# Optimization experiments

Measured on AMD Instinct MI355X. Metric: run time of the kernel, lower is better.

## Reference

```python
import jax, jax.numpy as jnp
import numpy as np


def setup_inputs() -> dict:
    key = jax.random.key(0)
    k1, k2 = jax.random.split(key)
    in_features, out_features, tokens = 4096, 4096, 8192
    x = jax.random.normal(k1, (tokens, in_features), dtype=jnp.float32)
    bound = 1.0 / np.sqrt(in_features)  # nn.Linear default init -> |W| <= 1
    W = jax.random.uniform(k2, (out_features, in_features), dtype=jnp.float32,
                           minval=-bound, maxval=bound)
    return {"x": x, "W": W}


def reference(x, W):
    # Forward of BinarizedLinear: y = x @ sign(W)^T (bias-free linear with
    # sign-binarized weights; the clamp_(-1,1) after sign() is a no-op).
    Wb = jnp.sign(W)  # [out, in], values in {-1, 0, +1}
    return jnp.einsum('ti,oi->to', x, Wb)  # [tokens, out]
```

## Files before the change

kernel.cpp:

```cpp
#include <hip/hip_runtime.h>
#include <hip/hip_bf16.h>
#include <stdint.h>

#define M_TOK 8192
#define N_OUT 4096
#define K_IN  4096

#define BM 256
#define BN 256
#define BKB 128
#define NT (K_IN / BKB)

typedef __attribute__((ext_vector_type(4))) int   i32x4;
typedef __attribute__((ext_vector_type(4))) float f32x4;

#define AS1 __attribute__((address_space(1)))
#define AS3 __attribute__((address_space(3)))
#define GLOAD_LDS16(g, l) \
  __builtin_amdgcn_global_load_lds((AS1 void*)(g), (AS3 void*)(l), 16, 0, 0)

#define BAR()     __builtin_amdgcn_s_barrier()
#define WAITALL() asm volatile("s_waitcnt vmcnt(0) lgkmcnt(0)" ::: "memory")
#define VMCNT8()  asm volatile("s_waitcnt vmcnt(8)" ::: "memory")
#define PRIO(p)   __builtin_amdgcn_s_setprio(p)
#define MFMAI8(a, b, c) __builtin_amdgcn_mfma_i32_16x16x64_i8((a), (b), (c), 0, 0, 0)

__global__ __launch_bounds__(256) void quant_x_i8(const float4* __restrict__ x,
                                                  int4* __restrict__ o,
                                                  float* __restrict__ scales) {
  const int row = blockIdx.x;
  const int t   = threadIdx.x;
  const float4* xr = x + (size_t)row * (K_IN / 4);
  float4 v[4];
  #pragma unroll
  for (int i = 0; i < 4; ++i) v[i] = xr[t * 4 + i];
  float m = 0.f;
  #pragma unroll
  for (int i = 0; i < 4; ++i)
    m = fmaxf(m, fmaxf(fmaxf(fabsf(v[i].x), fabsf(v[i].y)),
                       fmaxf(fabsf(v[i].z), fabsf(v[i].w))));
  #pragma unroll
  for (int off = 32; off; off >>= 1) m = fmaxf(m, __shfl_down(m, off));
  __shared__ float sm[4];
  if ((t & 63) == 0) sm[t >> 6] = m;
  __syncthreads();
  m = fmaxf(fmaxf(sm[0], sm[1]), fmaxf(sm[2], sm[3]));
  const float inv = m > 0.f ? 127.f / m : 0.f;
  if (t == 0) scales[row] = m > 0.f ? m / 127.f : 1.f;
  int q[4];
  #pragma unroll
  for (int i = 0; i < 4; ++i) {
    const int a0 = (int)rintf(v[i].x * inv);
    const int a1 = (int)rintf(v[i].y * inv);
    const int a2 = (int)rintf(v[i].z * inv);
    const int a3 = (int)rintf(v[i].w * inv);
    q[i] = (a0 & 255) | ((a1 & 255) << 8) | ((a2 & 255) << 16) | (a3 << 24);
  }
  o[(size_t)row * (K_IN / 16) + t] = make_int4(q[0], q[1], q[2], q[3]);
}

__global__ __launch_bounds__(256) void sgn_w_i8(const float4* __restrict__ w,
                                                int4* __restrict__ o, int n16) {
  int i = blockIdx.x * blockDim.x + threadIdx.x;
  int stride = gridDim.x * blockDim.x;
  for (; i < n16; i += stride) {
    int q[4];
    #pragma unroll
    for (int j = 0; j < 4; ++j) {
      float4 v = w[i * 4 + j];
      const int a0 = v.x > 0.f ? 1 : (v.x < 0.f ? -1 : 0);
      const int a1 = v.y > 0.f ? 1 : (v.y < 0.f ? -1 : 0);
      const int a2 = v.z > 0.f ? 1 : (v.z < 0.f ? -1 : 0);
      const int a3 = v.w > 0.f ? 1 : (v.w < 0.f ? -1 : 0);
      q[j] = (a0 & 255) | ((a1 & 255) << 8) | ((a2 & 255) << 16) | (a3 << 24);
    }
    o[i] = make_int4(q[0], q[1], q[2], q[3]);
  }
}

__global__ __launch_bounds__(512, 2) void bin_gemm_i8(const char* __restrict__ A,
                                                      const char* __restrict__ B,
                                                      const float* __restrict__ scales,
                                                      float* __restrict__ C) {
  __shared__ char lds[131072];

  const int tid  = threadIdx.x;
  const int w    = tid >> 6;
  const int lane = tid & 63;
  const int lr   = lane & 15;
  const int lk   = lane >> 4;
  const int wr   = w >> 2;
  const int wc   = w & 3;

  const int bm = blockIdx.x >> 4;
  const int bn = blockIdx.x & 15;

  const char* Ag = A + (size_t)bm * BM * K_IN;
  const char* Bg = B + (size_t)bn * BN * K_IN;

  const int c0 = w * 128 + lane;
  const int c1 = c0 + 64;
  const int r0 = c0 >> 3, r1 = c1 >> 3;
  const size_t g0 = (size_t)r0 * K_IN + (size_t)(((c0 ^ r0) & 7) << 4);
  const size_t g1 = (size_t)r1 * K_IN + (size_t)(((c1 ^ r1) & 7) << 4);
  const int ldsw = w * 128 * 16;

  auto stage = [&](int mat, int half, int tt) {
    const char* g = (mat ? Bg : Ag) + (size_t)half * (128 * K_IN)
                                    + (size_t)tt * BKB;
    char* l = &lds[((tt & 1) << 16) + (mat << 15) + (half << 14) + ldsw];
    GLOAD_LDS16(g + g0, l);
    GLOAD_LDS16(g + g1, l + 1024);
  };

  const int swz   = (lr & 7) << 4;
  const int a_row = (wr * 128 + lr) * 128;
  const int b_row = 32768 + (wc * 64 + lr) * 128;
  const int k0 = (lk * 16) ^ swz;
  const int k1 = (64 + lk * 16) ^ swz;

  i32x4 acc[8][4];
  #pragma unroll
  for (int m = 0; m < 8; ++m)
    #pragma unroll
    for (int n = 0; n < 4; ++n) { i32x4 z = {0, 0, 0, 0}; acc[m][n] = z; }

  stage(0, 0, 0); stage(0, 1, 0); stage(1, 0, 0); stage(1, 1, 0);
  stage(0, 0, 1); stage(0, 1, 1); stage(1, 0, 1); stage(1, 1, 1);
  VMCNT8();
  BAR();

  for (int t = 0; t < NT; ++t) {
    const char* L = &lds[(size_t)(t & 1) << 16];
    i32x4 aF[4][2], aS[4][2], bF[4][2];

    #pragma unroll
    for (int m = 0; m < 4; ++m) {
      aF[m][0] = *(const i32x4*)(L + a_row + m * 2048 + k0);
      aF[m][1] = *(const i32x4*)(L + a_row + m * 2048 + k1);
    }
    #pragma unroll
    for (int n = 0; n < 4; ++n) {
      bF[n][0] = *(const i32x4*)(L + b_row + n * 2048 + k0);
      bF[n][1] = *(const i32x4*)(L + b_row + n * 2048 + k1);
    }
    #pragma unroll
    for (int m = 0; m < 4; ++m) {
      aS[m][0] = *(const i32x4*)(L + a_row + 8192 + m * 2048 + k0);
      aS[m][1] = *(const i32x4*)(L + a_row + 8192 + m * 2048 + k1);
    }
    #pragma unroll
    for (int m = 0; m < 4; ++m)
      #pragma unroll
      for (int n = 0; n < 4; ++n) {
        acc[m][n] = MFMAI8(aF[m][0], bF[n][0], acc[m][n]);
        acc[m][n] = MFMAI8(aF[m][1], bF[n][1], acc[m][n]);
      }

    WAITALL();
    BAR();

    if (t + 2 < NT) {
      stage(1, 0, t + 2); stage(1, 1, t + 2);
      stage(0, 0, t + 2); stage(0, 1, t + 2);
    }
    PRIO(1);
    #pragma unroll
    for (int m = 0; m < 4; ++m)
      #pragma unroll
      for (int n = 0; n < 4; ++n) {
        acc[4 + m][n] = MFMAI8(aS[m][0], bF[n][0], acc[4 + m][n]);
        acc[4 + m][n] = MFMAI8(aS[m][1], bF[n][1], acc[4 + m][n]);
      }
    PRIO(0);
  }

  const int grow0 = bm * BM + wr * 128;
  float scl[8][4];
  #pragma unroll
  for (int m = 0; m < 8; ++m)
    #pragma unroll
    for (int j = 0; j < 4; ++j)
      scl[m][j] = scales[grow0 + m * 16 + lk * 4 + j];

  float* Cp = C + (size_t)grow0 * N_OUT + bn * BN + wc * 64;
  #pragma unroll
  for (int m = 0; m < 8; ++m)
    #pragma unroll
    for (int n = 0; n < 4; ++n)
      #pragma unroll
      for (int j = 0; j < 4; ++j)
        Cp[(size_t)(m * 16 + lk * 4 + j) * N_OUT + n * 16 + lr] =
            (float)acc[m][n][j] * scl[m][j];
}

__global__ __launch_bounds__(256) void fb_gemm(const float* __restrict__ x,
                                               const float* __restrict__ W,
                                               float* __restrict__ y) {
  __shared__ float xs[32][33];
  __shared__ float ws[32][33];
  const int bx = blockIdx.x;
  const int by = blockIdx.y;
  const int tx = threadIdx.x & 31;
  const int ty = threadIdx.x >> 5;
  float acc[4] = {0.f, 0.f, 0.f, 0.f};
  for (int k0 = 0; k0 < K_IN; k0 += 32) {
    #pragma unroll
    for (int i = 0; i < 4; ++i) {
      int r = ty + i * 8;
      xs[r][tx] = x[(size_t)(by * 32 + r) * K_IN + k0 + tx];
      float wv = W[(size_t)(bx * 32 + r) * K_IN + k0 + tx];
      ws[r][tx] = wv > 0.f ? 1.f : (wv < 0.f ? -1.f : 0.f);
    }
    __syncthreads();
    #pragma unroll
    for (int i = 0; i < 4; ++i) {
      int r = ty + i * 8;
      float s = acc[i];
      #pragma unroll
      for (int k = 0; k < 32; ++k) s += xs[r][k] * ws[tx][k];
      acc[i] = s;
    }
    __syncthreads();
  }
  #pragma unroll
  for (int i = 0; i < 4; ++i)
    y[(size_t)(by * 32 + ty + i * 8) * N_OUT + bx * 32 + tx] = acc[i];
}

extern "C" void kernel_launch(void* const* d_in, const int* in_sizes, int n_in,
                              void* d_out, int out_size, void* d_ws, size_t ws_size,
                              hipStream_t stream) {
  const float* x = (const float*)d_in[0];
  const float* W = (const float*)d_in[1];
  float* y = (float*)d_out;

  const size_t need = (size_t)M_TOK * K_IN + (size_t)N_OUT * K_IN
                    + (size_t)M_TOK * sizeof(float);
  if (ws_size >= need) {
    char*  xq = (char*)d_ws;
    char*  wq = xq + (size_t)M_TOK * K_IN;
    float* sc = (float*)(wq + (size_t)N_OUT * K_IN);
    quant_x_i8<<<M_TOK, 256, 0, stream>>>((const float4*)x, (int4*)xq, sc);
    sgn_w_i8<<<2048, 256, 0, stream>>>((const float4*)W, (int4*)wq,
                                       N_OUT * K_IN / 16);
    bin_gemm_i8<<<(M_TOK / BM) * (N_OUT / BN), 512, 0, stream>>>(xq, wq, sc, y);
  } else {
    dim3 g(N_OUT / 32, M_TOK / 32);
    fb_gemm<<<g, 256, 0, stream>>>(x, W, y);
  }
}
```

Before: 177.8 us.

## Software-pipeline LDS fragment loads across K halves and tiles in int8 GEMM

```diff
diff --git a/kernel.cpp b/kernel.cpp
--- a/kernel.cpp
+++ b/kernel.cpp
@@ -22,6 +22,8 @@
 #define BAR()     __builtin_amdgcn_s_barrier()
 #define WAITALL() asm volatile("s_waitcnt vmcnt(0) lgkmcnt(0)" ::: "memory")
 #define VMCNT8()  asm volatile("s_waitcnt vmcnt(8)" ::: "memory")
+#define LGKM12()  asm volatile("s_waitcnt lgkmcnt(12)" ::: "memory")
+#define SCHEDB()  __builtin_amdgcn_sched_barrier(0)
 #define PRIO(p)   __builtin_amdgcn_s_setprio(p)
 #define MFMAI8(a, b, c) __builtin_amdgcn_mfma_i32_16x16x64_i8((a), (b), (c), 0, 0, 0)
 
@@ -125,37 +127,37 @@
     #pragma unroll
     for (int n = 0; n < 4; ++n) { i32x4 z = {0, 0, 0, 0}; acc[m][n] = z; }
 
+  i32x4 aA[8], bA[4], aB[8], bB[4];
+
   stage(0, 0, 0); stage(0, 1, 0); stage(1, 0, 0); stage(1, 1, 0);
   stage(0, 0, 1); stage(0, 1, 1); stage(1, 0, 1); stage(1, 1, 1);
   VMCNT8();
   BAR();
+  {
+    const char* L0 = &lds[0];
+    #pragma unroll
+    for (int m = 0; m < 8; ++m) aA[m] = *(const i32x4*)(L0 + a_row + m * 2048 + k0);
+    #pragma unroll
+    for (int n = 0; n < 4; ++n) bA[n] = *(const i32x4*)(L0 + b_row + n * 2048 + k0);
+  }
 
   for (int t = 0; t < NT; ++t) {
-    const char* L = &lds[(size_t)(t & 1) << 16];
-    i32x4 aF[4][2], aS[4][2], bF[4][2];
-
-    #pragma unroll
-    for (int m = 0; m < 4; ++m) {
-      aF[m][0] = *(const i32x4*)(L + a_row + m * 2048 + k0);
-      aF[m][1] = *(const i32x4*)(L + a_row + m * 2048 + k1);
-    }
-    #pragma unroll
-    for (int n = 0; n < 4; ++n) {
-      bF[n][0] = *(const i32x4*)(L + b_row + n * 2048 + k0);
-      bF[n][1] = *(const i32x4*)(L + b_row + n * 2048 + k1);
-    }
-    #pragma unroll
-    for (int m = 0; m < 4; ++m) {
-      aS[m][0] = *(const i32x4*)(L + a_row + 8192 + m * 2048 + k0);
-      aS[m][1] = *(const i32x4*)(L + a_row + 8192 + m * 2048 + k1);
-    }
-    #pragma unroll
-    for (int m = 0; m < 4; ++m)
-      #pragma unroll
-      for (int n = 0; n < 4; ++n) {
-        acc[m][n] = MFMAI8(aF[m][0], bF[n][0], acc[m][n]);
-        acc[m][n] = MFMAI8(aF[m][1], bF[n][1], acc[m][n]);
-      }
+    const char* Lc = &lds[(size_t)(t & 1) << 16];
+    const char* Ln = &lds[(size_t)(~t & 1) << 16];
+
+    #pragma unroll
+    for (int m = 0; m < 8; ++m) aB[m] = *(const i32x4*)(Lc + a_row + m * 2048 + k1);
+    #pragma unroll
+    for (int n = 0; n < 4; ++n) bB[n] = *(const i32x4*)(Lc + b_row + n * 2048 + k1);
+    LGKM12();
+    SCHEDB();
+    PRIO(1);
+    #pragma unroll
+    for (int m = 0; m < 8; ++m)
+      #pragma unroll
+      for (int n = 0; n < 4; ++n)
+        acc[m][n] = MFMAI8(aA[m], bA[n], acc[m][n]);
+    PRIO(0);
 
     WAITALL();
     BAR();
@@ -164,14 +166,19 @@
       stage(1, 0, t + 2); stage(1, 1, t + 2);
       stage(0, 0, t + 2); stage(0, 1, t + 2);
     }
+    if (t + 1 < NT) {
+      #pragma unroll
+      for (int m = 0; m < 8; ++m) aA[m] = *(const i32x4*)(Ln + a_row + m * 2048 + k0);
+      #pragma unroll
+      for (int n = 0; n < 4; ++n) bA[n] = *(const i32x4*)(Ln + b_row + n * 2048 + k0);
+    }
+    SCHEDB();
     PRIO(1);
     #pragma unroll
-    for (int m = 0; m < 4; ++m)
-      #pragma unroll
-      for (int n = 0; n < 4; ++n) {
-        acc[4 + m][n] = MFMAI8(aS[m][0], bF[n][0], acc[4 + m][n]);
-        acc[4 + m][n] = MFMAI8(aS[m][1], bF[n][1], acc[4 + m][n]);
-      }
+    for (int m = 0; m < 8; ++m)
+      #pragma unroll
+      for (int n = 0; n < 4; ++n)
+        acc[m][n] = MFMAI8(aB[m], bB[n], acc[m][n]);
     PRIO(0);
   }
 
```

After: 180.2 us. About the same (+1.4%).

## Switch int8 GEMM to 32x32x32 MFMA with new LDS swizzle

Applied to the files above, without the earlier changes.

```diff
diff --git a/kernel.cpp b/kernel.cpp
--- a/kernel.cpp
+++ b/kernel.cpp
@@ -11,8 +11,8 @@
 #define BKB 128
 #define NT (K_IN / BKB)
 
-typedef __attribute__((ext_vector_type(4))) int   i32x4;
-typedef __attribute__((ext_vector_type(4))) float f32x4;
+typedef __attribute__((ext_vector_type(4)))  int i32x4;
+typedef __attribute__((ext_vector_type(16))) int i32x16;
 
 #define AS1 __attribute__((address_space(1)))
 #define AS3 __attribute__((address_space(3)))
@@ -23,7 +23,7 @@
 #define WAITALL() asm volatile("s_waitcnt vmcnt(0) lgkmcnt(0)" ::: "memory")
 #define VMCNT8()  asm volatile("s_waitcnt vmcnt(8)" ::: "memory")
 #define PRIO(p)   __builtin_amdgcn_s_setprio(p)
-#define MFMAI8(a, b, c) __builtin_amdgcn_mfma_i32_16x16x64_i8((a), (b), (c), 0, 0, 0)
+#define MFMA32I8(a, b, c) __builtin_amdgcn_mfma_i32_32x32x32_i8((a), (b), (c), 0, 0, 0)
 
 __global__ __launch_bounds__(256) void quant_x_i8(const float4* __restrict__ x,
                                                   int4* __restrict__ o,
@@ -87,8 +87,8 @@
   const int tid  = threadIdx.x;
   const int w    = tid >> 6;
   const int lane = tid & 63;
-  const int lr   = lane & 15;
-  const int lk   = lane >> 4;
+  const int l5   = lane & 31;
+  const int hi   = lane >> 5;
   const int wr   = w >> 2;
   const int wc   = w & 3;
 
@@ -101,9 +101,11 @@
   const int c0 = w * 128 + lane;
   const int c1 = c0 + 64;
   const int r0 = c0 >> 3, r1 = c1 >> 3;
-  const size_t g0 = (size_t)r0 * K_IN + (size_t)(((c0 ^ r0) & 7) << 4);
-  const size_t g1 = (size_t)r1 * K_IN + (size_t)(((c1 ^ r1) & 7) << 4);
-  const int ldsw = w * 128 * 16;
+  const size_t g0 = (size_t)r0 * K_IN
+                  + (size_t)((((c0 ^ r0) & 7) ^ ((r0 >> 3) & 3)) << 4);
+  const size_t g1 = (size_t)r1 * K_IN
+                  + (size_t)((((c1 ^ r1) & 7) ^ ((r1 >> 3) & 3)) << 4);
+  const int ldsw = w * 2048;
 
   auto stage = [&](int mat, int half, int tt) {
     const char* g = (mat ? Bg : Ag) + (size_t)half * (128 * K_IN)
@@ -113,17 +115,20 @@
     GLOAD_LDS16(g + g1, l + 1024);
   };
 
-  const int swz   = (lr & 7) << 4;
-  const int a_row = (wr * 128 + lr) * 128;
-  const int b_row = 32768 + (wc * 64 + lr) * 128;
-  const int k0 = (lk * 16) ^ swz;
-  const int k1 = (64 + lk * 16) ^ swz;
-
-  i32x4 acc[8][4];
-  #pragma unroll
-  for (int m = 0; m < 8; ++m)
-    #pragma unroll
-    for (int n = 0; n < 4; ++n) { i32x4 z = {0, 0, 0, 0}; acc[m][n] = z; }
+  const int fswz  = ((l5 & 7) ^ (l5 >> 3)) << 4;
+  const int a_row = (wr * 128 + l5) * 128;
+  const int b_row = 32768 + (wc * 64 + l5) * 128;
+  int kof[4];
+  #pragma unroll
+  for (int ks = 0; ks < 4; ++ks) kof[ks] = (ks * 32 + hi * 16) ^ fswz;
+
+  i32x16 acc[4][2];
+  #pragma unroll
+  for (int m = 0; m < 4; ++m)
+    #pragma unroll
+    for (int n = 0; n < 2; ++n)
+      #pragma unroll
+      for (int r = 0; r < 16; ++r) acc[m][n][r] = 0;
 
   stage(0, 0, 0); stage(0, 1, 0); stage(1, 0, 0); stage(1, 1, 0);
   stage(0, 0, 1); stage(0, 1, 1); stage(1, 0, 1); stage(1, 1, 1);
@@ -132,30 +137,27 @@
 
   for (int t = 0; t < NT; ++t) {
     const char* L = &lds[(size_t)(t & 1) << 16];
-    i32x4 aF[4][2], aS[4][2], bF[4][2];
-
-    #pragma unroll
-    for (int m = 0; m < 4; ++m) {
-      aF[m][0] = *(const i32x4*)(L + a_row + m * 2048 + k0);
-      aF[m][1] = *(const i32x4*)(L + a_row + m * 2048 + k1);
-    }
-    #pragma unroll
-    for (int n = 0; n < 4; ++n) {
-      bF[n][0] = *(const i32x4*)(L + b_row + n * 2048 + k0);
-      bF[n][1] = *(const i32x4*)(L + b_row + n * 2048 + k1);
-    }
-    #pragma unroll
-    for (int m = 0; m < 4; ++m) {
-      aS[m][0] = *(const i32x4*)(L + a_row + 8192 + m * 2048 + k0);
-      aS[m][1] = *(const i32x4*)(L + a_row + 8192 + m * 2048 + k1);
-    }
+    i32x4 aF[4][4], bF[2][4];
+
     #pragma unroll
     for (int m = 0; m < 4; ++m)
       #pragma unroll
-      for (int n = 0; n < 4; ++n) {
-        acc[m][n] = MFMAI8(aF[m][0], bF[n][0], acc[m][n]);
-        acc[m][n] = MFMAI8(aF[m][1], bF[n][1], acc[m][n]);
-      }
+      for (int ks = 0; ks < 4; ++ks)
+        aF[m][ks] = *(const i32x4*)(L + a_row + m * 4096 + kof[ks]);
+    #pragma unroll
+    for (int n = 0; n < 2; ++n)
+      #pragma unroll
+      for (int ks = 0; ks < 4; ++ks)
+        bF[n][ks] = *(const i32x4*)(L + b_row + n * 4096 + kof[ks]);
+    PRIO(1);
+    #pragma unroll
+    for (int m = 0; m < 2; ++m)
+      #pragma unroll
+      for (int n = 0; n < 2; ++n)
+        #pragma unroll
+        for (int ks = 0; ks < 4; ++ks)
+          acc[m][n] = MFMA32I8(aF[m][ks], bF[n][ks], acc[m][n]);
+    PRIO(0);
 
     WAITALL();
     BAR();
@@ -166,32 +168,26 @@
     }
     PRIO(1);
     #pragma unroll
-    for (int m = 0; m < 4; ++m)
-      #pragma unroll
-      for (int n = 0; n < 4; ++n) {
-        acc[4 + m][n] = MFMAI8(aS[m][0], bF[n][0], acc[4 + m][n]);
-        acc[4 + m][n] = MFMAI8(aS[m][1], bF[n][1], acc[4 + m][n]);
-      }
+    for (int m = 2; m < 4; ++m)
+      #pragma unroll
+      for (int n = 0; n < 2; ++n)
+        #pragma unroll
+        for (int ks = 0; ks < 4; ++ks)
+          acc[m][n] = MFMA32I8(aF[m][ks], bF[n][ks], acc[m][n]);
     PRIO(0);
   }
 
   const int grow0 = bm * BM + wr * 128;
-  float scl[8][4];
-  #pragma unroll
-  for (int m = 0; m < 8; ++m)
-    #pragma unroll
-    for (int j = 0; j < 4; ++j)
-      scl[m][j] = scales[grow0 + m * 16 + lk * 4 + j];
-
   float* Cp = C + (size_t)grow0 * N_OUT + bn * BN + wc * 64;
   #pragma unroll
-  for (int m = 0; m < 8; ++m)
-    #pragma unroll
-    for (int n = 0; n < 4; ++n)
-      #pragma unroll
-      for (int j = 0; j < 4; ++j)
-        Cp[(size_t)(m * 16 + lk * 4 + j) * N_OUT + n * 16 + lr] =
-            (float)acc[m][n][j] * scl[m][j];
+  for (int m = 0; m < 4; ++m)
+    #pragma unroll
+    for (int r = 0; r < 16; ++r) {
+      const int rowin = m * 32 + (r & 3) + 8 * (r >> 2) + 4 * hi;
+      const float s = scales[grow0 + rowin];
+      Cp[(size_t)rowin * N_OUT + l5]      = (float)acc[m][0][r] * s;
+      Cp[(size_t)rowin * N_OUT + 32 + l5] = (float)acc[m][1][r] * s;
+    }
 }
 
 __global__ __launch_bounds__(256) void fb_gemm(const float* __restrict__ x,
```

After: 189.2 us. 6.5% more time.
